# Optimization experiments

Measured on AMD Instinct MI355X. Metric: run time of the kernel, lower is better.

The kernel has to match this reference:

```python
import jax, jax.numpy as jnp
import numpy as np

K = 5        # kernel_size per dim
DIM = 3      # pseudo-coordinate dim
KTOT = K ** DIM   # 125 kernel weight matrices
S = 2 ** DIM      # 8 basis products for degree-1 open B-spline
KNN = 3


def spline_basis(ea):
    """Degree-1 open B-spline basis. ea: [E, DIM] in [0,1).
    Returns basis [E, S] and kernel weight indices wi [E, S]."""
    v = ea * (K - 1)
    b = jnp.floor(v)
    f = v - b                      # fractional part, grads flow here
    bi = b.astype(jnp.int32)
    bases, idxs = [], []
    for c in range(S):             # static loop over 2^DIM corner combos
        bs = jnp.ones(ea.shape[0], ea.dtype)
        wi = jnp.zeros(ea.shape[0], jnp.int32)
        for d in range(DIM):
            bit = (c >> d) & 1
            bs = bs * (f[:, d] if bit else 1.0 - f[:, d])
            wi = wi + jnp.clip(bi[:, d] + bit, 0, K - 1) * (K ** d)
        bases.append(bs)
        idxs.append(wi)
    return jnp.stack(bases, 1), jnp.stack(idxs, 1)


def spline_conv(x, src, dst, basis, wi, W, Wroot, bias):
    """SplineConv with aggr='mean', root weight and bias (PyG defaults)."""
    N, Cin = x.shape
    E = src.shape[0]
    xs = x[src]                                   # [E, Cin] gather
    vals = xs[:, None, :] * basis[:, :, None]     # [E, S, Cin]
    seg = (dst[:, None] * KTOT + wi).reshape(-1)  # bucket by (dst node, kernel)
    A = jax.ops.segment_sum(vals.reshape(-1, Cin), seg,
                            num_segments=N * KTOT).reshape(N, KTOT, Cin)
    out = jnp.einsum('nki,kio->no', A, W)         # apply kernel bank once
    deg = jax.ops.segment_sum(jnp.ones(E, x.dtype), dst, num_segments=N)
    out = out / jnp.maximum(deg, 1.0)[:, None]    # mean aggregation
    return out + x @ Wroot + bias


def knn_interpolate(x, pos_x, pos_y, batch_x, batch_y, k):
    """PyG knn_interpolate: inverse-squared-distance weighted k-NN average."""
    off = 1e5  # separate batches in coordinate space
    px = pos_x + batch_x[:, None].astype(pos_x.dtype) * off
    py = pos_y + batch_y[:, None].astype(pos_y.dtype) * off
    d2 = (jnp.sum(py ** 2, 1)[:, None] + jnp.sum(px ** 2, 1)[None, :]
          - 2.0 * (py @ px.T))                    # [Ny, Nx]
    negd, idx = jax.lax.top_k(-d2, k)             # k nearest
    w = 1.0 / jnp.maximum(-negd, 1e-16)           # [Ny, k]
    return (w[:, :, None] * x[idx]).sum(1) / w.sum(1)[:, None]


def setup_inputs() -> dict:
    key = jax.random.key(0)
    ks = jax.random.split(key, 12)
    N, E, Ny, C = 8192, 131072, 16384, 64
    return {
        'x': jax.random.normal(ks[0], (N, C), jnp.float32),
        'edge_index': jax.random.randint(ks[1], (2, E), 0, N, jnp.int32),
        'edge_attr': jax.random.uniform(ks[2], (E, DIM), jnp.float32),
        'pos_x': jax.random.normal(ks[3], (N, 3), jnp.float32),
        'batch_x': jnp.zeros((N,), jnp.int32),
        'pos_y': jax.random.normal(ks[4], (Ny, 3), jnp.float32),
        'batch_y': jnp.zeros((Ny,), jnp.int32),
        'Wa': jax.random.normal(ks[5], (KTOT, C, C), jnp.float32) * 0.05,
        'roota': jax.random.normal(ks[6], (C, C), jnp.float32) * 0.05,
        'biasa': jnp.zeros((C,), jnp.float32),
        'Wb': jax.random.normal(ks[7], (KTOT, C, C), jnp.float32) * 0.05,
        'rootb': jax.random.normal(ks[8], (C, C), jnp.float32) * 0.05,
        'biasb': jnp.zeros((C,), jnp.float32),
    }


def reference(x, edge_index, edge_attr, pos_x, batch_x, pos_y, batch_y,
              Wa, roota, biasa, Wb, rootb, biasb):
    src, dst = edge_index[0], edge_index[1]
    basis, wi = spline_basis(edge_attr)
    h = jax.nn.elu(spline_conv(x, src, dst, basis, wi, Wa, roota, biasa))
    h = jax.nn.elu(spline_conv(h, src, dst, basis, wi, Wb, rootb, biasb))
    return knn_interpolate(h, pos_x, pos_y, batch_x, batch_y, KNN)
```

## Files before the change

### kernel.cpp

```cpp
#include <hip/hip_runtime.h>
#include <hip/hip_bf16.h>
#include <math.h>

#define CDIV(a,b) (((a)+(b)-1)/(b))
#define WPCV 8
#define KCH 32

typedef __attribute__((ext_vector_type(8))) short bf16x8;
typedef __attribute__((ext_vector_type(4))) float f32x4;

__device__ __forceinline__ float elu_f(float x){ return x > 0.f ? x : expm1f(x); }
__device__ __forceinline__ unsigned short f2bf(float x){
    __hip_bfloat16 h = __float2bfloat16(x);
    union { __hip_bfloat16 b; unsigned short u; } cv; cv.b = h; return cv.u;
}
__device__ __forceinline__ float bf2f(unsigned short u){
    unsigned int ui = ((unsigned int)u) << 16;
    union { unsigned int u; float f; } cv; cv.u = ui; return cv.f;
}

__global__ void k_zero(int* __restrict__ p, int n)
{
    int i = blockIdx.x * blockDim.x + threadIdx.x;
    if (i < n) p[i] = 0;
}

__global__ void k_basis_px(const float* __restrict__ ea, const int* __restrict__ dst,
                        float* __restrict__ basis, int* __restrict__ cellid,
                        int* __restrict__ cellcnt, int* __restrict__ deg,
                        int* __restrict__ rank, int E, int EB, int PB,
                        const float* __restrict__ posx, const int* __restrict__ bx,
                        float4* __restrict__ px4, int N,
                        const float* __restrict__ x, unsigned short* __restrict__ xbf)
{
    const int tid = threadIdx.x;
    const int bid = blockIdx.x;
    if (bid >= EB) {
        int r = bid - EB;
        if (r < PB) {
            int n = r*256 + tid;
            if (n < N) {
                float off = (float)bx[n] * 1e5f;
                float a = posx[n*3+0]+off, b = posx[n*3+1]+off, c = posx[n*3+2]+off;
                px4[n] = make_float4(a, b, c, a*a + b*b + c*c);
            }
        } else {
            int i = (r - PB)*256 + tid;
            if (i < N*8) {
                const float4* xs = (const float4*)x + (size_t)i*2;
                float4 a4 = xs[0], b4 = xs[1];
                bf16x8 v;
                v[0]=(short)f2bf(a4.x); v[1]=(short)f2bf(a4.y);
                v[2]=(short)f2bf(a4.z); v[3]=(short)f2bf(a4.w);
                v[4]=(short)f2bf(b4.x); v[5]=(short)f2bf(b4.y);
                v[6]=(short)f2bf(b4.z); v[7]=(short)f2bf(b4.w);
                *(bf16x8*)(xbf + (size_t)i*8) = v;
            }
        }
        return;
    }
    __shared__ int hist[64];
    if (tid < 64) hist[tid] = 0;
    __syncthreads();
    int e = bid * 256 + tid;
    if (e < E) {
        float f[3]; int bi[3];
        #pragma unroll
        for (int d = 0; d < 3; d++) {
            float v = ea[e*3+d] * 4.f;
            float b = floorf(v);
            f[d] = v - b;
            int bb = (int)b; bb = bb < 0 ? 0 : (bb > 3 ? 3 : bb);
            bi[d] = bb;
        }
        int cell = bi[0] + 4*bi[1] + 16*bi[2];
        cellid[e] = cell;
        atomicAdd(&hist[cell], 1);
        rank[e] = atomicAdd(deg + dst[e], 1);
        float bs[8];
        #pragma unroll
        for (int c = 0; c < 8; c++) {
            float b = 1.f;
            #pragma unroll
            for (int d = 0; d < 3; d++)
                b *= ((c>>d)&1) ? f[d] : (1.f - f[d]);
            bs[c] = b;
        }
        float4* bw = (float4*)(basis + (size_t)e*8);
        bw[0] = make_float4(bs[0],bs[1],bs[2],bs[3]);
        bw[1] = make_float4(bs[4],bs[5],bs[6],bs[7]);
    }
    __syncthreads();
    if (tid < 64 && hist[tid]) atomicAdd(cellcnt + tid, hist[tid]);
}

__global__ __launch_bounds__(1024) void k_degscan(const int* __restrict__ deg,
                        int* __restrict__ csr, float* __restrict__ invdeg, int N,
                        const int* __restrict__ cellcnt, int* __restrict__ cellstart,
                        int* __restrict__ cellfill)
{
    __shared__ int buf[2][1024];
    const int t = threadIdx.x;
    if (t < 64) {
        int v = cellcnt[t];
        int s = v;
        #pragma unroll
        for (int off = 1; off < 64; off <<= 1) {
            int o = __shfl_up(s, off, 64);
            if (t >= off) s += o;
        }
        cellstart[t] = s - v; cellfill[t] = s - v;
        if (t == 63) cellstart[64] = s;
    }
    const int base = t*8;
    int loc[8]; int s = 0;
    #pragma unroll
    for (int j = 0; j < 8; j++) {
        loc[j] = s;
        int d = (base+j < N) ? deg[base+j] : 0;
        if (base+j < N) invdeg[base+j] = 1.f / fmaxf((float)d, 1.f);
        s += d;
    }
    buf[0][t] = s; __syncthreads();
    int pb = 0;
    for (int off = 1; off < 1024; off <<= 1) {
        int v = buf[pb][t];
        if (t >= off) v += buf[pb][t-off];
        buf[pb^1][t] = v; __syncthreads(); pb ^= 1;
    }
    int excl = buf[pb][t] - s;
    #pragma unroll
    for (int j = 0; j < 8; j++)
        if (base+j < N) csr[base+j] = excl + loc[j];
    if (t == 0) csr[N] = buf[pb][1023];
}

__global__ __launch_bounds__(256) void k_pack(
    const int* __restrict__ cellid, int* __restrict__ fill, int* __restrict__ elist,
    const int* __restrict__ dst, const int* __restrict__ rank,
    const int* __restrict__ csr, int* __restrict__ dstpos, int E, int SB,
    const float* __restrict__ Wa, const float* __restrict__ Wb,
    unsigned short* __restrict__ WTa, unsigned short* __restrict__ WTb)
{
    __shared__ float shbuf[64*65];
    const int tid = threadIdx.x;
    const int bid = blockIdx.x;
    if (bid < SB) {
        int* hist = (int*)shbuf;
        int* bas  = hist + 64;
        if (tid < 64) hist[tid] = 0;
        __syncthreads();
        int e = bid * 256 + tid;
        int cell = 0, loc = 0;
        bool act = e < E;
        if (act) { cell = cellid[e]; loc = atomicAdd(&hist[cell], 1); }
        __syncthreads();
        if (tid < 64) bas[tid] = hist[tid] ? atomicAdd(fill + tid, hist[tid]) : 0;
        __syncthreads();
        if (act) elist[bas[cell] + loc] = e;
    } else if (bid < 2*SB) {
        int e = (bid - SB) * 256 + tid;
        if (e < E) dstpos[e] = csr[dst[e]] + rank[e];
    } else {
        int b = bid - 2*SB;
        float (*ws65)[65] = (float(*)[65])shbuf;
        const float* Wsrc = (b < 125) ? (Wa + (size_t)b*4096) : (Wb + (size_t)(b-125)*4096);
        unsigned short* Wdst = (b < 125) ? (WTa + (size_t)b*4096) : (WTb + (size_t)(b-125)*4096);
        #pragma unroll
        for (int j = 0; j < 16; j++) {
            int idx = j*256 + tid;
            ws65[idx>>6][idx&63] = Wsrc[idx];
        }
        __syncthreads();
        #pragma unroll
        for (int j = 0; j < 16; j++) {
            int idx = j*256 + tid;
            int o = idx>>6, i = idx&63;
            Wdst[idx] = f2bf(ws65[i][o]);
        }
    }
}

__global__ __launch_bounds__(256) void k_conv(
    const unsigned short* __restrict__ xin, const unsigned short* __restrict__ WT,
    const int* __restrict__ elist, const int* __restrict__ cellstart,
    const float* __restrict__ basis, const int* __restrict__ src,
    const int* __restrict__ dstpos, unsigned short* __restrict__ ye)
{
    __shared__ unsigned short wt[8][64][64];
    __shared__ unsigned short xb[64][64];
    __shared__ float bts[8][64];
    __shared__ int dpos[64];

    const int cell = blockIdx.x / WPCV;
    const int sub  = blockIdx.x % WPCV;
    const int tid  = threadIdx.x;
    const int w    = tid >> 6;
    const int lane = tid & 63;
    const int eh   = w >> 1;
    const int oh   = w & 1;
    const int l15  = lane & 15;
    const int kgrp = lane >> 4;
    const int swz  = lane & 7;

    int kc[8];
    {
        int b0 = cell & 3, b1 = (cell >> 2) & 3, b2 = (cell >> 4) & 3;
        #pragma unroll
        for (int c = 0; c < 8; c++)
            kc[c] = (b0 + (c&1)) + 5*(b1 + ((c>>1)&1)) + 25*(b2 + ((c>>2)&1));
    }

    #pragma unroll
    for (int j = 0; j < 16; j++) {
        int cj  = j >> 1;
        int off = ((j & 1) << 8) + tid;
        int row = off >> 3, colc = off & 7;
        bf16x8 v = ((const bf16x8*)(WT + (size_t)kc[cj]*4096))[off];
        *(bf16x8*)&wt[cj][row][(colc ^ (row & 7)) << 3] = v;
    }

    const int s0 = cellstart[cell], s1 = cellstart[cell+1];
    const int se = tid >> 2, sm = tid & 3;

    for (int base = s0 + sub*64; base < s1; base += WPCV*64) {
        int ne = s1 - base; ne = ne > 64 ? 64 : ne;
        __syncthreads();
        int c0 = (sm*2)     ^ (se & 7);
        int c1 = (sm*2 + 1) ^ (se & 7);
        if (se < ne) {
            int eid = elist[base + se];
            int sn  = src[eid];
            const bf16x8* xr = (const bf16x8*)(xin + (size_t)sn*64);
            bf16x8 v0 = xr[sm*2], v1 = xr[sm*2+1];
            *(bf16x8*)&xb[se][c0 << 3] = v0;
            *(bf16x8*)&xb[se][c1 << 3] = v1;
            if (sm == 0) {
                const float4* br = (const float4*)(basis + (size_t)eid*8);
                float4 bA = br[0], bB = br[1];
                bts[0][se]=bA.x; bts[1][se]=bA.y; bts[2][se]=bA.z; bts[3][se]=bA.w;
                bts[4][se]=bB.x; bts[5][se]=bB.y; bts[6][se]=bB.z; bts[7][se]=bB.w;
                dpos[se] = dstpos[eid];
            }
        } else {
            bf16x8 z = {0,0,0,0,0,0,0,0};
            *(bf16x8*)&xb[se][c0 << 3] = z;
            *(bf16x8*)&xb[se][c1 << 3] = z;
            if (sm == 0) dpos[se] = -1;
        }
        __syncthreads();

        bf16x8 a[2][2];
        #pragma unroll
        for (int me = 0; me < 2; me++) {
            int arow = eh*32 + me*16 + l15;
            #pragma unroll
            for (int kh = 0; kh < 2; kh++)
                a[me][kh] = *(const bf16x8*)&xb[arow][((kh*4 + kgrp) ^ swz) << 3];
        }

        f32x4 y[2][2] = {{{0,0,0,0},{0,0,0,0}},{{0,0,0,0},{0,0,0,0}}};
        #pragma unroll
        for (int c = 0; c < 8; c++) {
            float4 bv[2];
            bv[0] = *(const float4*)&bts[c][eh*32 +      (kgrp << 2)];
            bv[1] = *(const float4*)&bts[c][eh*32 + 16 + (kgrp << 2)];
            bf16x8 bfr[2][2];
            #pragma unroll
            for (int nb = 0; nb < 2; nb++) {
                int brow = oh*32 + nb*16 + l15;
                #pragma unroll
                for (int kh = 0; kh < 2; kh++)
                    bfr[nb][kh] = *(const bf16x8*)&wt[c][brow][((kh*4 + kgrp) ^ swz) << 3];
            }
            #pragma unroll
            for (int me = 0; me < 2; me++) {
                #pragma unroll
                for (int nb = 0; nb < 2; nb++) {
                    f32x4 t = {0.f, 0.f, 0.f, 0.f};
                    t = __builtin_amdgcn_mfma_f32_16x16x32_bf16(a[me][0], bfr[nb][0], t, 0, 0, 0);
                    t = __builtin_amdgcn_mfma_f32_16x16x32_bf16(a[me][1], bfr[nb][1], t, 0, 0, 0);
                    y[me][nb][0] = fmaf(bv[me].x, t[0], y[me][nb][0]);
                    y[me][nb][1] = fmaf(bv[me].y, t[1], y[me][nb][1]);
                    y[me][nb][2] = fmaf(bv[me].z, t[2], y[me][nb][2]);
                    y[me][nb][3] = fmaf(bv[me].w, t[3], y[me][nb][3]);
                }
            }
        }
        #pragma unroll
        for (int me = 0; me < 2; me++) {
            #pragma unroll
            for (int r = 0; r < 4; r++) {
                int el = eh*32 + me*16 + (kgrp << 2) + r;
                int dp = dpos[el];
                if (dp >= 0) {
                    unsigned short* yp = ye + (size_t)dp*64 + oh*32 + l15;
                    yp[0]  = f2bf(y[me][0][r]);
                    yp[16] = f2bf(y[me][1][r]);
                }
            }
        }
    }
}

__global__ __launch_bounds__(256) void k_gather_knn(
    const unsigned short* __restrict__ ye, const int* __restrict__ csr,
    const unsigned short* __restrict__ xin, const float* __restrict__ root,
    const float* __restrict__ bias, const float* __restrict__ invdeg,
    unsigned short* __restrict__ hout, int N, int KB,
    const float4* __restrict__ px4, const float* __restrict__ posy,
    const int* __restrict__ by, float* __restrict__ pd, int* __restrict__ pi,
    int Npts, int Ny, int chbase)
{
    __shared__ float sh[4][64];
    const int bid = blockIdx.x;
    const int tid = threadIdx.x;

    if (bid < KB) {
        const int qb  = (bid / 16) * 256;
        const int ch  = chbase + (bid % 16);
        const int NC  = Npts / KCH;
        const int q = qb + tid;
        float off = (float)by[q] * 1e5f;
        float qa = posy[q*3+0]+off, qbv = posy[q*3+1]+off, qc = posy[q*3+2]+off;
        float sy = qa*qa + qbv*qbv + qc*qc;
        float qa2 = -2.f*qa, qb2 = -2.f*qbv, qc2 = -2.f*qc;

        const float4* __restrict__ pts = px4 + (size_t)ch * NC;
        const int gbase = ch * NC;

        float d0 = 3.4e38f, d1 = 3.4e38f, d2s = 3.4e38f;
        int   i0 = 0x7fffffff, i1 = 0x7fffffff, i2 = 0x7fffffff;
        #pragma unroll 16
        for (int p = 0; p < NC; p++) {
            float4 pt = pts[p];
            float u  = fmaf(qa2, pt.x, fmaf(qb2, pt.y, fmaf(qc2, pt.z, sy + pt.w)));
            int   gi = gbase + p;
            bool c0 = u < d0, c1 = u < d1, c2 = u < d2s;
            float nd0 = fminf(d0, u);
            float nd1 = __builtin_amdgcn_fmed3f(d0, u, d1);
            float nd2 = __builtin_amdgcn_fmed3f(u, d1, d2s);
            i2 = c1 ? i1 : (c2 ? gi : i2);
            i1 = c0 ? i0 : (c1 ? gi : i1);
            i0 = c0 ? gi : i0;
            d0 = nd0; d1 = nd1; d2s = nd2;
        }
        size_t ob = ((size_t)ch*Ny + q)*3;
        pd[ob+0]=d0; pd[ob+1]=d1; pd[ob+2]=d2s;
        pi[ob+0]=i0; pi[ob+1]=i1; pi[ob+2]=i2;
        return;
    }

    const int w = tid >> 6, lane = tid & 63;
    const int n = (bid - KB)*4 + w;
    if (n >= N) return;
    const int s0 = csr[n], s1 = csr[n+1];
    const int j8 = lane >> 3, c8 = lane & 7;
    float acc[8] = {};
    for (int base = s0; base < s1; base += 8) {
        int ei = base + j8;
        if (ei < s1) {
            bf16x8 v = *(const bf16x8*)(ye + (size_t)ei*64 + c8*8);
            #pragma unroll
            for (int k = 0; k < 8; k++)
                acc[k] += bf2f((unsigned short)v[k]);
        }
    }
    #pragma unroll
    for (int m = 8; m <= 32; m <<= 1) {
        #pragma unroll
        for (int k = 0; k < 8; k++)
            acc[k] += __shfl_xor(acc[k], m, 64);
    }
    if (j8 == 0) {
        #pragma unroll
        for (int k = 0; k < 8; k++) sh[w][c8*8+k] = acc[k];
    }
    float aggr = sh[w][lane];
    float av = aggr * invdeg[n];
    float xv = bf2f(xin[(size_t)n*64 + lane]);
    float rt = bias[lane];
    #pragma unroll 8
    for (int i = 0; i < 64; i++)
        rt = fmaf(__shfl(xv, i, 64), root[i*64 + lane], rt);
    hout[(size_t)n*64 + lane] = f2bf(elu_f(av + rt));
}

__global__ __launch_bounds__(256) void k_knn_merge(
    const float* __restrict__ pd, const int* __restrict__ pi,
    const unsigned short* __restrict__ h2, float* __restrict__ out, int Ny)
{
    const int w = threadIdx.x >> 6, lane = threadIdx.x & 63;
    const int q = blockIdx.x*4 + w;
    float a0 = 3.4e38f, a1 = 3.4e38f, a2 = 3.4e38f;
    int   b0 = 0x7fffffff, b1 = 0x7fffffff, b2 = 0x7fffffff;
    if (lane < KCH) {
        size_t base = ((size_t)lane*Ny + q)*3;
        a0 = pd[base+0]; a1 = pd[base+1]; a2 = pd[base+2];
        b0 = pi[base+0]; b1 = pi[base+1]; b2 = pi[base+2];
    }
    float rd[3]; int ri[3];
    #pragma unroll
    for (int j = 0; j < 3; j++) {
        float md = a0; int mi = b0;
        #pragma unroll
        for (int s = 1; s < 64; s <<= 1) {
            float od = __shfl_xor(md, s, 64);
            int   oi = __shfl_xor(mi, s, 64);
            if (od < md || (od == md && oi < mi)) { md = od; mi = oi; }
        }
        rd[j] = md; ri[j] = mi;
        if (b0 == mi) { a0=a1; b0=b1; a1=a2; b1=b2; a2=3.4e38f; b2=0x7fffffff; }
    }
    float w0 = 1.f/fmaxf(rd[0], 1e-16f);
    float w1 = 1.f/fmaxf(rd[1], 1e-16f);
    float w2 = 1.f/fmaxf(rd[2], 1e-16f);
    float ws = w0 + w1 + w2;
    float v = w0*bf2f(h2[(size_t)ri[0]*64+lane]) + w1*bf2f(h2[(size_t)ri[1]*64+lane])
            + w2*bf2f(h2[(size_t)ri[2]*64+lane]);
    out[(size_t)q*64+lane] = v / ws;
}

extern "C" void kernel_launch(void* const* d_in, const int* in_sizes, int n_in,
                              void* d_out, int out_size, void* d_ws, size_t ws_size,
                              hipStream_t stream)
{
    const float* x     = (const float*)d_in[0];
    const int*   ei    = (const int*)d_in[1];
    const float* ea    = (const float*)d_in[2];
    const float* posx  = (const float*)d_in[3];
    const int*   bx    = (const int*)d_in[4];
    const float* posy  = (const float*)d_in[5];
    const int*   by    = (const int*)d_in[6];
    const float* Wa    = (const float*)d_in[7];
    const float* roota = (const float*)d_in[8];
    const float* biasa = (const float*)d_in[9];
    const float* Wb    = (const float*)d_in[10];
    const float* rootb = (const float*)d_in[11];
    const float* biasb = (const float*)d_in[12];

    const int N  = in_sizes[0] / 64;
    const int E  = in_sizes[1] / 2;
    const int Ny = in_sizes[5] / 3;
    const int* srcp = ei;
    const int* dstp = ei + E;

    char* ws = (char*)d_ws;
    size_t off = 0;
    auto alloc = [&](size_t bytes) { void* p = ws + off; off += (bytes + 255) & ~255ull; return p; };
    float*  basis    = (float*)alloc((size_t)E*8*4);
    int*    cellid   = (int*)  alloc((size_t)E*4);
    int*    rank     = (int*)  alloc((size_t)E*4);
    int*    elist    = (int*)  alloc((size_t)E*4);
    int*    dstpos   = (int*)  alloc((size_t)E*4);
    int*    deg      = (int*)  alloc((size_t)N*4);
    int*    cellcnt  = (int*)  alloc(64*4);
    int*    csr      = (int*)  alloc((size_t)(N+1)*4);
    float*  invdeg   = (float*)alloc((size_t)N*4);
    int*    cellstart= (int*)  alloc(65*4);
    int*    cellfill = (int*)  alloc(64*4);
    unsigned short* xbf = (unsigned short*)alloc((size_t)N*64*2);
    unsigned short* h1  = (unsigned short*)alloc((size_t)N*64*2);
    unsigned short* h2  = (unsigned short*)alloc((size_t)N*64*2);
    float4* px4      = (float4*)alloc((size_t)N*16);
    unsigned short* WTa = (unsigned short*)alloc((size_t)125*4096*2);
    unsigned short* WTb = (unsigned short*)alloc((size_t)125*4096*2);
    unsigned short* ye  = (unsigned short*)alloc((size_t)E*64*2);
    float* pd = (float*)alloc((size_t)Ny*KCH*3*4);
    int*   pi = (int*)  alloc((size_t)Ny*KCH*3*4);
    (void)ws_size; (void)n_in; (void)out_size;

    const int EB = CDIV(E,256);
    const int PB = CDIV(N,256);
    const int XB = CDIV(N*8,256);
    const int GB = CDIV(N,4);
    const int KB = (Ny/256)*16;
    const int ZN = N + 64;

    k_zero    <<<CDIV(ZN,256), 256, 0, stream>>>(deg, ZN);
    k_basis_px<<<EB+PB+XB, 256, 0, stream>>>(ea, dstp, basis, cellid, cellcnt, deg, rank,
                                             E, EB, PB, posx, bx, px4, N, x, xbf);
    k_degscan <<<1, 1024, 0, stream>>>(deg, csr, invdeg, N, cellcnt, cellstart, cellfill);
    k_pack    <<<2*EB + 250, 256, 0, stream>>>(cellid, cellfill, elist, dstp, rank,
                                               csr, dstpos, E, EB, Wa, Wb, WTa, WTb);

    k_conv      <<<64*WPCV, 256, 0, stream>>>(xbf, WTa, elist, cellstart, basis, srcp, dstpos, ye);
    k_gather_knn<<<KB+GB, 256, 0, stream>>>(ye, csr, xbf, roota, biasa, invdeg, h1, N, KB,
                                            px4, posy, by, pd, pi, N, Ny, 0);

    k_conv      <<<64*WPCV, 256, 0, stream>>>(h1, WTb, elist, cellstart, basis, srcp, dstpos, ye);
    k_gather_knn<<<KB+GB, 256, 0, stream>>>(ye, csr, h1, rootb, biasb, invdeg, h2, N, KB,
                                            px4, posy, by, pd, pi, N, Ny, 16);

    k_knn_merge<<<Ny/4, 256, 0, stream>>>(pd, pi, h2, (float*)d_out, Ny);
}
```

Baseline: 165.5 us.

## Halve conv weight LDS, raise blocks per cell, move weight transpose earlier

Cuts the k_conv shared weight buffer from 8 to 4 kernel matrices. The two halves of the 8 corner weights are now reloaded from global memory into LDS for every 64-edge chunk, which lowers LDS per block so more blocks fit per CU. Blocks per cell rise from 8 to 12. The weight transpose to bf16 moves from k_pack into k_basis_px, so k_pack gets lighter and needs less shared memory. The cost is repeated weight loads per chunk and extra barriers inside the loop.

```diff
diff --git a/kernel.cpp b/kernel.cpp
--- a/kernel.cpp
+++ b/kernel.cpp
@@ -3,7 +3,7 @@
 #include <math.h>
 
 #define CDIV(a,b) (((a)+(b)-1)/(b))
-#define WPCV 8
+#define WPCV 12
 #define KCH 32
 
 typedef __attribute__((ext_vector_type(8))) short bf16x8;
@@ -28,11 +28,14 @@
 __global__ void k_basis_px(const float* __restrict__ ea, const int* __restrict__ dst,
                         float* __restrict__ basis, int* __restrict__ cellid,
                         int* __restrict__ cellcnt, int* __restrict__ deg,
-                        int* __restrict__ rank, int E, int EB, int PB,
+                        int* __restrict__ rank, int E, int EB, int PB, int XB,
                         const float* __restrict__ posx, const int* __restrict__ bx,
                         float4* __restrict__ px4, int N,
-                        const float* __restrict__ x, unsigned short* __restrict__ xbf)
-{
+                        const float* __restrict__ x, unsigned short* __restrict__ xbf,
+                        const float* __restrict__ Wa, const float* __restrict__ Wb,
+                        unsigned short* __restrict__ WTa, unsigned short* __restrict__ WTb)
+{
+    __shared__ float shbuf[64*65];
     const int tid = threadIdx.x;
     const int bid = blockIdx.x;
     if (bid >= EB) {
@@ -44,7 +47,7 @@
                 float a = posx[n*3+0]+off, b = posx[n*3+1]+off, c = posx[n*3+2]+off;
                 px4[n] = make_float4(a, b, c, a*a + b*b + c*c);
             }
-        } else {
+        } else if (r < PB + XB) {
             int i = (r - PB)*256 + tid;
             if (i < N*8) {
                 const float4* xs = (const float4*)x + (size_t)i*2;
@@ -56,10 +59,27 @@
                 v[6]=(short)f2bf(b4.z); v[7]=(short)f2bf(b4.w);
                 *(bf16x8*)(xbf + (size_t)i*8) = v;
             }
+        } else {
+            int b = r - PB - XB;
+            float (*ws65)[65] = (float(*)[65])shbuf;
+            const float* Wsrc = (b < 125) ? (Wa + (size_t)b*4096) : (Wb + (size_t)(b-125)*4096);
+            unsigned short* Wdst = (b < 125) ? (WTa + (size_t)b*4096) : (WTb + (size_t)(b-125)*4096);
+            #pragma unroll
+            for (int j = 0; j < 16; j++) {
+                int idx = j*256 + tid;
+                ws65[idx>>6][idx&63] = Wsrc[idx];
+            }
+            __syncthreads();
+            #pragma unroll
+            for (int j = 0; j < 16; j++) {
+                int idx = j*256 + tid;
+                int o = idx>>6, i = idx&63;
+                Wdst[idx] = f2bf(ws65[i][o]);
+            }
         }
         return;
     }
-    __shared__ int hist[64];
+    int* hist = (int*)shbuf;
     if (tid < 64) hist[tid] = 0;
     __syncthreads();
     int e = bid * 256 + tid;
@@ -138,16 +158,12 @@
 __global__ __launch_bounds__(256) void k_pack(
     const int* __restrict__ cellid, int* __restrict__ fill, int* __restrict__ elist,
     const int* __restrict__ dst, const int* __restrict__ rank,
-    const int* __restrict__ csr, int* __restrict__ dstpos, int E, int SB,
-    const float* __restrict__ Wa, const float* __restrict__ Wb,
-    unsigned short* __restrict__ WTa, unsigned short* __restrict__ WTb)
-{
-    __shared__ float shbuf[64*65];
+    const int* __restrict__ csr, int* __restrict__ dstpos, int E, int SB)
+{
+    __shared__ int hist[64], bas[64];
     const int tid = threadIdx.x;
     const int bid = blockIdx.x;
     if (bid < SB) {
-        int* hist = (int*)shbuf;
-        int* bas  = hist + 64;
         if (tid < 64) hist[tid] = 0;
         __syncthreads();
         int e = bid * 256 + tid;
@@ -158,26 +174,9 @@
         if (tid < 64) bas[tid] = hist[tid] ? atomicAdd(fill + tid, hist[tid]) : 0;
         __syncthreads();
         if (act) elist[bas[cell] + loc] = e;
-    } else if (bid < 2*SB) {
+    } else {
         int e = (bid - SB) * 256 + tid;
         if (e < E) dstpos[e] = csr[dst[e]] + rank[e];
-    } else {
-        int b = bid - 2*SB;
-        float (*ws65)[65] = (float(*)[65])shbuf;
-        const float* Wsrc = (b < 125) ? (Wa + (size_t)b*4096) : (Wb + (size_t)(b-125)*4096);
-        unsigned short* Wdst = (b < 125) ? (WTa + (size_t)b*4096) : (WTb + (size_t)(b-125)*4096);
-        #pragma unroll
-        for (int j = 0; j < 16; j++) {
-            int idx = j*256 + tid;
-            ws65[idx>>6][idx&63] = Wsrc[idx];
-        }
-        __syncthreads();
-        #pragma unroll
-        for (int j = 0; j < 16; j++) {
-            int idx = j*256 + tid;
-            int o = idx>>6, i = idx&63;
-            Wdst[idx] = f2bf(ws65[i][o]);
-        }
     }
 }
 
@@ -187,7 +186,7 @@
     const float* __restrict__ basis, const int* __restrict__ src,
     const int* __restrict__ dstpos, unsigned short* __restrict__ ye)
 {
-    __shared__ unsigned short wt[8][64][64];
+    __shared__ unsigned short wt[4][64][64];
     __shared__ unsigned short xb[64][64];
     __shared__ float bts[8][64];
     __shared__ int dpos[64];
@@ -209,15 +208,6 @@
         #pragma unroll
         for (int c = 0; c < 8; c++)
             kc[c] = (b0 + (c&1)) + 5*(b1 + ((c>>1)&1)) + 25*(b2 + ((c>>2)&1));
-    }
-
-    #pragma unroll
-    for (int j = 0; j < 16; j++) {
-        int cj  = j >> 1;
-        int off = ((j & 1) << 8) + tid;
-        int row = off >> 3, colc = off & 7;
-        bf16x8 v = ((const bf16x8*)(WT + (size_t)kc[cj]*4096))[off];
-        *(bf16x8*)&wt[cj][row][(colc ^ (row & 7)) << 3] = v;
     }
 
     const int s0 = cellstart[cell], s1 = cellstart[cell+1];
@@ -248,6 +238,14 @@
             *(bf16x8*)&xb[se][c1 << 3] = z;
             if (sm == 0) dpos[se] = -1;
         }
+        #pragma unroll
+        for (int j = 0; j < 8; j++) {
+            int cj  = j >> 1;
+            int off = ((j & 1) << 8) + tid;
+            int row = off >> 3, colc = off & 7;
+            bf16x8 v = ((const bf16x8*)(WT + (size_t)kc[cj]*4096))[off];
+            *(bf16x8*)&wt[cj][row][(colc ^ (row & 7)) << 3] = v;
+        }
         __syncthreads();
 
         bf16x8 a[2][2];
@@ -261,7 +259,7 @@
 
         f32x4 y[2][2] = {{{0,0,0,0},{0,0,0,0}},{{0,0,0,0},{0,0,0,0}}};
         #pragma unroll
-        for (int c = 0; c < 8; c++) {
+        for (int c = 0; c < 4; c++) {
             float4 bv[2];
             bv[0] = *(const float4*)&bts[c][eh*32 +      (kgrp << 2)];
             bv[1] = *(const float4*)&bts[c][eh*32 + 16 + (kgrp << 2)];
@@ -272,6 +270,43 @@
                 #pragma unroll
                 for (int kh = 0; kh < 2; kh++)
                     bfr[nb][kh] = *(const bf16x8*)&wt[c][brow][((kh*4 + kgrp) ^ swz) << 3];
+            }
+            #pragma unroll
+            for (int me = 0; me < 2; me++) {
+                #pragma unroll
+                for (int nb = 0; nb < 2; nb++) {
+                    f32x4 t = {0.f, 0.f, 0.f, 0.f};
+                    t = __builtin_amdgcn_mfma_f32_16x16x32_bf16(a[me][0], bfr[nb][0], t, 0, 0, 0);
+                    t = __builtin_amdgcn_mfma_f32_16x16x32_bf16(a[me][1], bfr[nb][1], t, 0, 0, 0);
+                    y[me][nb][0] = fmaf(bv[me].x, t[0], y[me][nb][0]);
+                    y[me][nb][1] = fmaf(bv[me].y, t[1], y[me][nb][1]);
+                    y[me][nb][2] = fmaf(bv[me].z, t[2], y[me][nb][2]);
+                    y[me][nb][3] = fmaf(bv[me].w, t[3], y[me][nb][3]);
+                }
+            }
+        }
+        __syncthreads();
+        #pragma unroll
+        for (int j = 0; j < 8; j++) {
+            int cj  = j >> 1;
+            int off = ((j & 1) << 8) + tid;
+            int row = off >> 3, colc = off & 7;
+            bf16x8 v = ((const bf16x8*)(WT + (size_t)kc[4 + cj]*4096))[off];
+            *(bf16x8*)&wt[cj][row][(colc ^ (row & 7)) << 3] = v;
+        }
+        __syncthreads();
+        #pragma unroll
+        for (int c = 4; c < 8; c++) {
+            float4 bv[2];
+            bv[0] = *(const float4*)&bts[c][eh*32 +      (kgrp << 2)];
+            bv[1] = *(const float4*)&bts[c][eh*32 + 16 + (kgrp << 2)];
+            bf16x8 bfr[2][2];
+            #pragma unroll
+            for (int nb = 0; nb < 2; nb++) {
+                int brow = oh*32 + nb*16 + l15;
+                #pragma unroll
+                for (int kh = 0; kh < 2; kh++)
+                    bfr[nb][kh] = *(const bf16x8*)&wt[c-4][brow][((kh*4 + kgrp) ^ swz) << 3];
             }
             #pragma unroll
             for (int me = 0; me < 2; me++) {
@@ -478,11 +513,12 @@
     const int ZN = N + 64;
 
     k_zero    <<<CDIV(ZN,256), 256, 0, stream>>>(deg, ZN);
-    k_basis_px<<<EB+PB+XB, 256, 0, stream>>>(ea, dstp, basis, cellid, cellcnt, deg, rank,
-                                             E, EB, PB, posx, bx, px4, N, x, xbf);
+    k_basis_px<<<EB+PB+XB+250, 256, 0, stream>>>(ea, dstp, basis, cellid, cellcnt, deg, rank,
+                                             E, EB, PB, XB, posx, bx, px4, N, x, xbf,
+                                             Wa, Wb, WTa, WTb);
     k_degscan <<<1, 1024, 0, stream>>>(deg, csr, invdeg, N, cellcnt, cellstart, cellfill);
-    k_pack    <<<2*EB + 250, 256, 0, stream>>>(cellid, cellfill, elist, dstp, rank,
-                                               csr, dstpos, E, EB, Wa, Wb, WTa, WTb);
+    k_pack    <<<2*EB, 256, 0, stream>>>(cellid, cellfill, elist, dstp, rank,
+                                         csr, dstpos, E, EB);
 
     k_conv      <<<64*WPCV, 256, 0, stream>>>(xbf, WTa, elist, cellstart, basis, srcp, dstpos, ye);
     k_gather_knn<<<KB+GB, 256, 0, stream>>>(ye, csr, xbf, roota, biasa, invdeg, h1, N, KB,
```

New measurement: 197.9 us. 19.6% more time.

## Keep conv weight fragments in registers and move weight transpose earlier

Applied to the files above, without the earlier changes.

The conv kernel no longer stages the eight 64x64 bf16 weight tiles in shared memory. Each wave loads its own MFMA B-operand fragments straight from global memory into registers once, and the launch bound now asks for 2 blocks per SM. This removes 64KB of LDS per block and the per-iteration LDS reads for weights, at the cost of many more registers (wreg holds 32 bf16x8 values) and possible spills. The weight transpose and bf16 conversion blocks also move from k_pack into k_basis_px, so that work overlaps the earlier basis pass.

```diff
diff --git a/kernel.cpp b/kernel.cpp
--- a/kernel.cpp
+++ b/kernel.cpp
@@ -28,11 +28,14 @@
 __global__ void k_basis_px(const float* __restrict__ ea, const int* __restrict__ dst,
                         float* __restrict__ basis, int* __restrict__ cellid,
                         int* __restrict__ cellcnt, int* __restrict__ deg,
-                        int* __restrict__ rank, int E, int EB, int PB,
+                        int* __restrict__ rank, int E, int EB, int PB, int XB,
                         const float* __restrict__ posx, const int* __restrict__ bx,
                         float4* __restrict__ px4, int N,
-                        const float* __restrict__ x, unsigned short* __restrict__ xbf)
-{
+                        const float* __restrict__ x, unsigned short* __restrict__ xbf,
+                        const float* __restrict__ Wa, const float* __restrict__ Wb,
+                        unsigned short* __restrict__ WTa, unsigned short* __restrict__ WTb)
+{
+    __shared__ float shbuf[64*65];
     const int tid = threadIdx.x;
     const int bid = blockIdx.x;
     if (bid >= EB) {
@@ -44,7 +47,7 @@
                 float a = posx[n*3+0]+off, b = posx[n*3+1]+off, c = posx[n*3+2]+off;
                 px4[n] = make_float4(a, b, c, a*a + b*b + c*c);
             }
-        } else {
+        } else if (r < PB + XB) {
             int i = (r - PB)*256 + tid;
             if (i < N*8) {
                 const float4* xs = (const float4*)x + (size_t)i*2;
@@ -56,10 +59,27 @@
                 v[6]=(short)f2bf(b4.z); v[7]=(short)f2bf(b4.w);
                 *(bf16x8*)(xbf + (size_t)i*8) = v;
             }
+        } else {
+            int b = r - PB - XB;
+            float (*ws65)[65] = (float(*)[65])shbuf;
+            const float* Wsrc = (b < 125) ? (Wa + (size_t)b*4096) : (Wb + (size_t)(b-125)*4096);
+            unsigned short* Wdst = (b < 125) ? (WTa + (size_t)b*4096) : (WTb + (size_t)(b-125)*4096);
+            #pragma unroll
+            for (int j = 0; j < 16; j++) {
+                int idx = j*256 + tid;
+                ws65[idx>>6][idx&63] = Wsrc[idx];
+            }
+            __syncthreads();
+            #pragma unroll
+            for (int j = 0; j < 16; j++) {
+                int idx = j*256 + tid;
+                int o = idx>>6, i = idx&63;
+                Wdst[idx] = f2bf(ws65[i][o]);
+            }
         }
         return;
     }
-    __shared__ int hist[64];
+    int* hist = (int*)shbuf;
     if (tid < 64) hist[tid] = 0;
     __syncthreads();
     int e = bid * 256 + tid;
@@ -138,16 +158,12 @@
 __global__ __launch_bounds__(256) void k_pack(
     const int* __restrict__ cellid, int* __restrict__ fill, int* __restrict__ elist,
     const int* __restrict__ dst, const int* __restrict__ rank,
-    const int* __restrict__ csr, int* __restrict__ dstpos, int E, int SB,
-    const float* __restrict__ Wa, const float* __restrict__ Wb,
-    unsigned short* __restrict__ WTa, unsigned short* __restrict__ WTb)
-{
-    __shared__ float shbuf[64*65];
+    const int* __restrict__ csr, int* __restrict__ dstpos, int E, int SB)
+{
+    __shared__ int hist[64], bas[64];
     const int tid = threadIdx.x;
     const int bid = blockIdx.x;
     if (bid < SB) {
-        int* hist = (int*)shbuf;
-        int* bas  = hist + 64;
         if (tid < 64) hist[tid] = 0;
         __syncthreads();
         int e = bid * 256 + tid;
@@ -158,36 +174,18 @@
         if (tid < 64) bas[tid] = hist[tid] ? atomicAdd(fill + tid, hist[tid]) : 0;
         __syncthreads();
         if (act) elist[bas[cell] + loc] = e;
-    } else if (bid < 2*SB) {
+    } else {
         int e = (bid - SB) * 256 + tid;
         if (e < E) dstpos[e] = csr[dst[e]] + rank[e];
-    } else {
-        int b = bid - 2*SB;
-        float (*ws65)[65] = (float(*)[65])shbuf;
-        const float* Wsrc = (b < 125) ? (Wa + (size_t)b*4096) : (Wb + (size_t)(b-125)*4096);
-        unsigned short* Wdst = (b < 125) ? (WTa + (size_t)b*4096) : (WTb + (size_t)(b-125)*4096);
-        #pragma unroll
-        for (int j = 0; j < 16; j++) {
-            int idx = j*256 + tid;
-            ws65[idx>>6][idx&63] = Wsrc[idx];
-        }
-        __syncthreads();
-        #pragma unroll
-        for (int j = 0; j < 16; j++) {
-            int idx = j*256 + tid;
-            int o = idx>>6, i = idx&63;
-            Wdst[idx] = f2bf(ws65[i][o]);
-        }
-    }
-}
-
-__global__ __launch_bounds__(256) void k_conv(
+    }
+}
+
+__global__ __launch_bounds__(256, 2) void k_conv(
     const unsigned short* __restrict__ xin, const unsigned short* __restrict__ WT,
     const int* __restrict__ elist, const int* __restrict__ cellstart,
     const float* __restrict__ basis, const int* __restrict__ src,
     const int* __restrict__ dstpos, unsigned short* __restrict__ ye)
 {
-    __shared__ unsigned short wt[8][64][64];
     __shared__ unsigned short xb[64][64];
     __shared__ float bts[8][64];
     __shared__ int dpos[64];
@@ -211,13 +209,17 @@
             kc[c] = (b0 + (c&1)) + 5*(b1 + ((c>>1)&1)) + 25*(b2 + ((c>>2)&1));
     }
 
+    bf16x8 wreg[8][2][2];
     #pragma unroll
-    for (int j = 0; j < 16; j++) {
-        int cj  = j >> 1;
-        int off = ((j & 1) << 8) + tid;
-        int row = off >> 3, colc = off & 7;
-        bf16x8 v = ((const bf16x8*)(WT + (size_t)kc[cj]*4096))[off];
-        *(bf16x8*)&wt[cj][row][(colc ^ (row & 7)) << 3] = v;
+    for (int c = 0; c < 8; c++) {
+        const unsigned short* Wk = WT + (size_t)kc[c]*4096;
+        #pragma unroll
+        for (int nb = 0; nb < 2; nb++) {
+            int brow = oh*32 + nb*16 + l15;
+            #pragma unroll
+            for (int kh = 0; kh < 2; kh++)
+                wreg[c][nb][kh] = *(const bf16x8*)(Wk + brow*64 + (kh*4 + kgrp)*8);
+        }
     }
 
     const int s0 = cellstart[cell], s1 = cellstart[cell+1];
@@ -265,21 +267,13 @@
             float4 bv[2];
             bv[0] = *(const float4*)&bts[c][eh*32 +      (kgrp << 2)];
             bv[1] = *(const float4*)&bts[c][eh*32 + 16 + (kgrp << 2)];
-            bf16x8 bfr[2][2];
-            #pragma unroll
-            for (int nb = 0; nb < 2; nb++) {
-                int brow = oh*32 + nb*16 + l15;
-                #pragma unroll
-                for (int kh = 0; kh < 2; kh++)
-                    bfr[nb][kh] = *(const bf16x8*)&wt[c][brow][((kh*4 + kgrp) ^ swz) << 3];
-            }
             #pragma unroll
             for (int me = 0; me < 2; me++) {
                 #pragma unroll
                 for (int nb = 0; nb < 2; nb++) {
                     f32x4 t = {0.f, 0.f, 0.f, 0.f};
-                    t = __builtin_amdgcn_mfma_f32_16x16x32_bf16(a[me][0], bfr[nb][0], t, 0, 0, 0);
-                    t = __builtin_amdgcn_mfma_f32_16x16x32_bf16(a[me][1], bfr[nb][1], t, 0, 0, 0);
+                    t = __builtin_amdgcn_mfma_f32_16x16x32_bf16(a[me][0], wreg[c][nb][0], t, 0, 0, 0);
+                    t = __builtin_amdgcn_mfma_f32_16x16x32_bf16(a[me][1], wreg[c][nb][1], t, 0, 0, 0);
                     y[me][nb][0] = fmaf(bv[me].x, t[0], y[me][nb][0]);
                     y[me][nb][1] = fmaf(bv[me].y, t[1], y[me][nb][1]);
                     y[me][nb][2] = fmaf(bv[me].z, t[2], y[me][nb][2]);
@@ -478,11 +472,12 @@
     const int ZN = N + 64;
 
     k_zero    <<<CDIV(ZN,256), 256, 0, stream>>>(deg, ZN);
-    k_basis_px<<<EB+PB+XB, 256, 0, stream>>>(ea, dstp, basis, cellid, cellcnt, deg, rank,
-                                             E, EB, PB, posx, bx, px4, N, x, xbf);
+    k_basis_px<<<EB+PB+XB+250, 256, 0, stream>>>(ea, dstp, basis, cellid, cellcnt, deg, rank,
+                                             E, EB, PB, XB, posx, bx, px4, N, x, xbf,
+                                             Wa, Wb, WTa, WTb);
     k_degscan <<<1, 1024, 0, stream>>>(deg, csr, invdeg, N, cellcnt, cellstart, cellfill);
-    k_pack    <<<2*EB + 250, 256, 0, stream>>>(cellid, cellfill, elist, dstp, rank,
-                                               csr, dstpos, E, EB, Wa, Wb, WTa, WTb);
+    k_pack    <<<2*EB, 256, 0, stream>>>(cellid, cellfill, elist, dstp, rank,
+                                         csr, dstpos, E, EB);
 
     k_conv      <<<64*WPCV, 256, 0, stream>>>(xbf, WTa, elist, cellstart, basis, srcp, dstpos, ye);
     k_gather_knn<<<KB+GB, 256, 0, stream>>>(ye, csr, xbf, roota, biasa, invdeg, h1, N, KB,
```

After: 428.2 us. 2.59x slower.
